# Performance work log

Measured on AMD Instinct MI355X. Metric: run time of the kernel, lower is better.

The kernel has to match this reference:

```python
import jax, jax.numpy as jnp
import numpy as np

N = 50000   # nodes
E = 800000  # edges (avg degree 16)
D = 128     # dim (in == out per layer)
R = 8       # num_relations
B = 4       # num_bases
L = 2       # conv_layer_num
EPS = 1e-5      # LayerNorm eps
SLOPE = 0.2     # leaky_relu negative slope


def setup_inputs() -> dict:
    key = jax.random.key(0)
    ks = jax.random.split(key, 10)
    s = 0.05
    x = jax.random.normal(ks[0], (N, D), dtype=jnp.float32)
    edge_index = jax.random.randint(ks[1], (2, E), 0, N)
    edge_type = jax.random.randint(ks[2], (E,), 0, R)
    basis = jax.random.normal(ks[3], (L, B, D, D), dtype=jnp.float32) * s
    att_r = jax.random.normal(ks[4], (L, R, B), dtype=jnp.float32) * s
    att = jax.random.normal(ks[5], (L, 2 * D), dtype=jnp.float32) * s
    root = jax.random.normal(ks[6], (L, D, D), dtype=jnp.float32) * s
    bias = jax.random.normal(ks[7], (L, D), dtype=jnp.float32) * s
    ln_w = jnp.ones((L, D), dtype=jnp.float32)
    ln_b = jnp.zeros((L, D), dtype=jnp.float32)
    return {"x": x, "edge_index": edge_index, "edge_type": edge_type,
            "basis": basis, "att_r": att_r, "att": att, "root": root,
            "bias": bias, "ln_w": ln_w, "ln_b": ln_b}


def _gnn_layer(x, src, dst, et, basis, att_r, att, root, bias, ln_w, ln_b):
    # relation weights from bases: [R, D, D]
    w = jnp.einsum('rb,bio->rio', att_r, basis)
    # transform all nodes under all relations once, then gather per edge
    xw = jnp.einsum('ni,rio->rno', x, w)          # [R, N, D]
    x_j = xw[et, src]                              # [E, D] relation-specific src msg
    xr = x @ root                                  # [N, D] root transform
    x_i = xr[dst]                                  # [E, D]
    # attention: (cat[x_i, x_j] * att).sum(-1), leaky_relu, segment softmax by dst
    alpha = x_i @ att[:D] + x_j @ att[D:]          # [E]
    alpha = jnp.where(alpha > 0, alpha, SLOPE * alpha)
    amax = jax.ops.segment_max(alpha, dst, num_segments=N)
    amax = jnp.where(jnp.isfinite(amax), amax, 0.0)
    ex = jnp.exp(alpha - amax[dst])
    denom = jax.ops.segment_sum(ex, dst, num_segments=N)
    alpha = ex / (denom[dst] + 1e-16)
    # weighted scatter-add aggregation (dropout rate = 0 -> identity)
    aggr = jax.ops.segment_sum(x_j * alpha[:, None], dst, num_segments=N)  # [N, D]
    out = aggr + xr + bias
    # LayerNorm
    mu = out.mean(-1, keepdims=True)
    var = out.var(-1, keepdims=True)
    out = (out - mu) / jnp.sqrt(var + EPS) * ln_w + ln_b
    return jnp.tanh(out)


def reference(x, edge_index, edge_type, basis, att_r, att, root, bias, ln_w, ln_b):
    src, dst = edge_index[0], edge_index[1]
    states = []
    for l in range(L):
        x = _gnn_layer(x, src, dst, edge_type, basis[l], att_r[l], att[l],
                       root[l], bias[l], ln_w[l], ln_b[l])
        states.append(x)
    return (x, jnp.stack(states))
```

## Files before the change

kernel.cpp:

```cpp
#include <hip/hip_runtime.h>
#include <math.h>

#define D 128
#define NB 4
#define NR 8
#define NLAYER 2
#define KTOT 640
#define EPSV 1e-5f
#define SLOPE 0.2f

typedef __attribute__((ext_vector_type(8))) short short8;
typedef __attribute__((ext_vector_type(4))) float f32x4;

__device__ __forceinline__ unsigned short f2bf(float f) {
  unsigned u = __float_as_uint(f);
  u += 0x7FFF + ((u >> 16) & 1);
  return (unsigned short)(u >> 16);
}

__device__ __forceinline__ float block_sum_128(float v, volatile float* scratch) {
#pragma unroll
  for (int off = 32; off > 0; off >>= 1) v += __shfl_xor(v, off);
  __syncthreads();
  if ((threadIdx.x & 63) == 0) scratch[threadIdx.x >> 6] = v;
  __syncthreads();
  return scratch[0] + scratch[1];
}

__global__ void hist_kernel(const int* __restrict__ dst, int* __restrict__ deg, int E) {
  int e = blockIdx.x * 256 + threadIdx.x;
  if (e < E) atomicAdd(&deg[dst[e]], 1);
}

__global__ void __launch_bounds__(1024) scan_kernel(const int* __restrict__ deg,
                                                    int* __restrict__ offs,
                                                    int* __restrict__ cur, int n) {
  __shared__ int wsums[16];
  const int tid = threadIdx.x, lane = tid & 63, wid = tid >> 6;
  int carry = 0;
  for (int base = 0; base < n; base += 4096) {
    int i0 = base + tid * 4;
    int v0 = 0, v1 = 0, v2 = 0, v3 = 0;
    if (i0 + 3 < n) {
      int4 q = *(const int4*)(deg + i0);
      v0 = q.x; v1 = q.y; v2 = q.z; v3 = q.w;
    } else if (i0 < n) {
      v0 = deg[i0];
      if (i0 + 1 < n) v1 = deg[i0 + 1];
      if (i0 + 2 < n) v2 = deg[i0 + 2];
    }
    int tsum = v0 + v1 + v2 + v3;
    int x = tsum;
#pragma unroll
    for (int off = 1; off < 64; off <<= 1) {
      int y = __shfl_up(x, off);
      if (lane >= off) x += y;
    }
    if (lane == 63) wsums[wid] = x;
    __syncthreads();
    if (wid == 0) {
      int ws = (lane < 16) ? wsums[lane] : 0;
#pragma unroll
      for (int off = 1; off < 16; off <<= 1) {
        int y = __shfl_up(ws, off);
        if (lane >= off) ws += y;
      }
      if (lane < 16) wsums[lane] = ws;
    }
    __syncthreads();
    int prefix = carry + ((wid > 0) ? wsums[wid - 1] : 0) + x - tsum;
    int e0 = prefix, e1 = e0 + v0, e2 = e1 + v1, e3 = e2 + v2;
    if (i0 < n)     { offs[i0] = e0;     cur[i0] = e0; }
    if (i0 + 1 < n) { offs[i0 + 1] = e1; cur[i0 + 1] = e1; }
    if (i0 + 2 < n) { offs[i0 + 2] = e2; cur[i0 + 2] = e2; }
    if (i0 + 3 < n) { offs[i0 + 3] = e3; cur[i0 + 3] = e3; }
    int btot = wsums[15];
    __syncthreads();
    carry += btot;
  }
  if (tid == 0) offs[n] = carry;
}

__global__ void scatter_kernel(const int* __restrict__ src, const int* __restrict__ dst,
                               const int* __restrict__ et, int* __restrict__ cur,
                               unsigned* __restrict__ csr, int E) {
  int e = blockIdx.x * 256 + threadIdx.x;
  if (e < E) {
    int d = dst[e];
    int pos = atomicAdd(&cur[d], 1);
    csr[pos] = (unsigned)src[e] | ((unsigned)et[e] << 16);
  }
}

__global__ void __launch_bounds__(128) prep_w(const float* __restrict__ basis,
                                              const float* __restrict__ root,
                                              const float* __restrict__ att,
                                              unsigned short* __restrict__ BT0,
                                              unsigned short* __restrict__ BT1,
                                              float* __restrict__ av0, float* __restrict__ av1) {
  __shared__ float scratch[2];
  int k = blockIdx.x, l = 0;
  if (k >= KTOT) { k -= KTOT; l = 1; }
  const float* basis_l = basis + (size_t)l * NB * D * D;
  const float* root_l  = root + (size_t)l * D * D;
  const float* att_l   = att + (size_t)l * 2 * D;
  unsigned short* BT = l ? BT1 : BT0;
  float* av = l ? av1 : av0;
  const int o = threadIdx.x;
  float v = (k < 512) ? basis_l[(size_t)(k >> 7) * (D * D) + (size_t)(k & 127) * D + o]
                      : root_l[(size_t)(k - 512) * D + o];
  BT[(size_t)o * KTOT + k] = f2bf(v);
  float w = (k < 512) ? att_l[D + o] : att_l[o];
  float s = block_sum_128(v * w, scratch);
  if (o == 0) av[k] = s;
}

__global__ void prep_x(const float* __restrict__ x0, unsigned short* __restrict__ ga, int N) {
  int n = blockIdx.x, c = threadIdx.x;
  float v = (n < N) ? x0[(size_t)n * D + c] : 0.f;
  ga[(size_t)n * KTOT + 512 + c] = f2bf(v);
}

__global__ void __launch_bounds__(256) a2_kernel(const unsigned short* __restrict__ ga,
                                                 const float* __restrict__ av,
                                                 float* __restrict__ ai,
                                                 float* __restrict__ ajb, int N) {
  int n = blockIdx.x * 4 + (threadIdx.x >> 6);
  int lane = threadIdx.x & 63;
  if (n >= N) return;
  unsigned xv = *(const unsigned*)(ga + (size_t)n * KTOT + 512 + 2 * lane);
  float x0 = __uint_as_float(xv << 16);
  float x1 = __uint_as_float(xv & 0xFFFF0000u);
  float d[5];
#pragma unroll
  for (int b = 0; b < 4; ++b) {
    float2 w = *(const float2*)(av + b * D + 2 * lane);
    d[b] = x0 * w.x + x1 * w.y;
  }
  {
    float2 w = *(const float2*)(av + 512 + 2 * lane);
    d[4] = x0 * w.x + x1 * w.y;
  }
#pragma unroll
  for (int off = 1; off < 64; off <<= 1) {
#pragma unroll
    for (int i = 0; i < 5; ++i) d[i] += __shfl_xor(d[i], off);
  }
  if (lane == 0) {
    *(float4*)(ajb + (size_t)n * 4) = make_float4(d[0], d[1], d[2], d[3]);
    ai[n] = d[4];
  }
}

__global__ void __launch_bounds__(256) node_flash(
    unsigned short* __restrict__ ga, const float* __restrict__ ai, const float* __restrict__ ajb,
    const int* __restrict__ offs, const unsigned* __restrict__ csr,
    const float* __restrict__ attr_l, int N) {
  __shared__ float s_c[NR * NB];
  __shared__ float4 s_wc[4][64];
  __shared__ unsigned s_pk[4][64];
  const int w = threadIdx.x >> 6, lane = threadIdx.x & 63;
  const int n = blockIdx.x * 4 + w;
  if (lane < NR * NB) s_c[lane] = attr_l[lane];
  if (n >= N) return;
  const int b0 = offs[n], b1 = offs[n + 1];
  const float ain = ai[n];
  float m = -INFINITY, ssum = 0.f;
  float acc[4][2] = {};
  for (int cb = b0; cb < b1; cb += 64) {
    int cnt = min(64, b1 - cb);
    float alpha = -INFINITY;
    unsigned pk = 0;
    float4 cv = make_float4(0.f, 0.f, 0.f, 0.f);
    if (lane < cnt) {
      pk = csr[cb + lane];
      unsigned sn = pk & 0xFFFFu, rt = pk >> 16;
      float4 aj = *(const float4*)(ajb + (size_t)sn * 4);
      cv = *(const float4*)(&s_c[rt * 4]);
      float a = ain + cv.x * aj.x + cv.y * aj.y + cv.z * aj.z + cv.w * aj.w;
      alpha = a > 0.f ? a : SLOPE * a;
    }
    float cmax = alpha;
#pragma unroll
    for (int off = 32; off > 0; off >>= 1) cmax = fmaxf(cmax, __shfl_xor(cmax, off));
    float nm = fmaxf(m, cmax);
    float ex = (lane < cnt) ? __expf(alpha - nm) : 0.f;
    float csum = ex;
#pragma unroll
    for (int off = 32; off > 0; off >>= 1) csum += __shfl_xor(csum, off);
    float f = __expf(m - nm);
    ssum = ssum * f + csum;
#pragma unroll
    for (int b = 0; b < 4; ++b) { acc[b][0] *= f; acc[b][1] *= f; }
    m = nm;
    s_pk[w][lane] = pk;
    s_wc[w][lane] = make_float4(ex * cv.x, ex * cv.y, ex * cv.z, ex * cv.w);
#pragma unroll 2
    for (int j = 0; j < cnt; ++j) {
      float4 wc = s_wc[w][j];
      unsigned sn = s_pk[w][j] & 0xFFFFu;
      unsigned xv = *(const unsigned*)(ga + (size_t)sn * KTOT + 512 + 2 * lane);
      float x0 = __uint_as_float(xv << 16);
      float x1 = __uint_as_float(xv & 0xFFFF0000u);
      acc[0][0] = fmaf(wc.x, x0, acc[0][0]); acc[0][1] = fmaf(wc.x, x1, acc[0][1]);
      acc[1][0] = fmaf(wc.y, x0, acc[1][0]); acc[1][1] = fmaf(wc.y, x1, acc[1][1]);
      acc[2][0] = fmaf(wc.z, x0, acc[2][0]); acc[2][1] = fmaf(wc.z, x1, acc[2][1]);
      acc[3][0] = fmaf(wc.w, x0, acc[3][0]); acc[3][1] = fmaf(wc.w, x1, acc[3][1]);
    }
  }
  float inv = 1.f / (ssum + 1e-16f);
  unsigned short* gp = ga + (size_t)n * KTOT;
#pragma unroll
  for (int b = 0; b < 4; ++b) {
    unsigned r = (unsigned)f2bf(acc[b][0] * inv) | ((unsigned)f2bf(acc[b][1] * inv) << 16);
    *(unsigned*)(gp + b * D + 2 * lane) = r;
  }
}

__global__ void __launch_bounds__(256) gemm2_kernel(
    unsigned short* __restrict__ ga, const unsigned short* __restrict__ BT,
    const float* __restrict__ bias_l, const float* __restrict__ lnw_l,
    const float* __restrict__ lnb_l, float* __restrict__ st,
    float* __restrict__ xfinal, int n_nodes) {
  __shared__ unsigned short sB[128 * 72];
  const int tid = threadIdx.x;
  const int wv = tid >> 6, lane = tid & 63;
  const int l15 = lane & 15, quad = lane >> 4;
  const int rowb = blockIdx.x * 64 + wv * 16;
  const unsigned short* garow = ga + (size_t)(rowb + l15) * KTOT;
  f32x4 acc[8];
  const f32x4 zero = {0.f, 0.f, 0.f, 0.f};
#pragma unroll
  for (int ct = 0; ct < 8; ++ct) acc[ct] = zero;
#pragma unroll
  for (int ch = 0; ch < 10; ++ch) {
    const int k0 = ch * 64;
    short8 a[2];
#pragma unroll
    for (int kc = 0; kc < 2; ++kc)
      a[kc] = *(const short8*)(garow + k0 + kc * 32 + quad * 8);
    __syncthreads();
#pragma unroll
    for (int p = 0; p < 4; ++p) {
      int idx = p * 256 + tid;
      int col = idx >> 3, k8 = idx & 7;
      *(short8*)(sB + col * 72 + k8 * 8) =
          *(const short8*)(BT + (size_t)col * KTOT + k0 + k8 * 8);
    }
    __syncthreads();
#pragma unroll
    for (int kc = 0; kc < 2; ++kc) {
#pragma unroll
      for (int ct = 0; ct < 8; ++ct) {
        const short8* b = (const short8*)(sB + (ct * 16 + l15) * 72 + kc * 32 + quad * 8);
        acc[ct] = __builtin_amdgcn_mfma_f32_16x16x32_bf16(a[kc], *b, acc[ct], 0, 0, 0);
      }
    }
  }
  const int r0 = rowb + quad * 4;
  float bia[8], lw[8], lb[8];
#pragma unroll
  for (int ct = 0; ct < 8; ++ct) {
    int col = ct * 16 + l15;
    bia[ct] = bias_l[col]; lw[ct] = lnw_l[col]; lb[ct] = lnb_l[col];
  }
  float vsum[4] = {0.f, 0.f, 0.f, 0.f}, vsq[4] = {0.f, 0.f, 0.f, 0.f};
#pragma unroll
  for (int ct = 0; ct < 8; ++ct) {
#pragma unroll
    for (int r = 0; r < 4; ++r) {
      float v = acc[ct][r] + bia[ct];
      acc[ct][r] = v;
      vsum[r] += v; vsq[r] += v * v;
    }
  }
#pragma unroll
  for (int r = 0; r < 4; ++r) {
#pragma unroll
    for (int off = 1; off < 16; off <<= 1) {
      vsum[r] += __shfl_xor(vsum[r], off);
      vsq[r]  += __shfl_xor(vsq[r], off);
    }
  }
  float mu[4], rs[4];
#pragma unroll
  for (int r = 0; r < 4; ++r) {
    mu[r] = vsum[r] * (1.0f / D);
    float var = vsq[r] * (1.0f / D) - mu[r] * mu[r];
    rs[r] = rsqrtf(var + EPSV);
  }
#pragma unroll
  for (int ct = 0; ct < 8; ++ct) {
#pragma unroll
    for (int r = 0; r < 4; ++r) {
      int row = r0 + r;
      if (row >= n_nodes) continue;
      int col = ct * 16 + l15;
      float nv = (acc[ct][r] - mu[r]) * rs[r] * lw[ct] + lb[ct];
      float val = tanhf(nv);
      st[(size_t)row * D + col] = val;
      if (xfinal) xfinal[(size_t)row * D + col] = val;
      ga[(size_t)row * KTOT + 512 + col] = f2bf(val);
    }
  }
}

extern "C" void kernel_launch(void* const* d_in, const int* in_sizes, int n_in,
                              void* d_out, int out_size, void* d_ws, size_t ws_size,
                              hipStream_t stream) {
  const float* x0    = (const float*)d_in[0];
  const int*   ei    = (const int*)d_in[1];
  const int*   etype = (const int*)d_in[2];
  const float* basis = (const float*)d_in[3];
  const float* att_r = (const float*)d_in[4];
  const float* att   = (const float*)d_in[5];
  const float* root  = (const float*)d_in[6];
  const float* bias  = (const float*)d_in[7];
  const float* lnw   = (const float*)d_in[8];
  const float* lnb   = (const float*)d_in[9];
  float* out = (float*)d_out;
  const int N = in_sizes[0] / D;
  const int E = in_sizes[2];
  const int Npad = ((N + 63) / 64) * 64;

  char* p = (char*)d_ws;
  auto alloc = [&](size_t bytes) { void* r = (void*)p; p += (bytes + 255) & ~(size_t)255; return r; };
  unsigned short* ga   = (unsigned short*)alloc((size_t)Npad * KTOT * 2);
  unsigned short* BT0  = (unsigned short*)alloc((size_t)D * KTOT * 2);
  unsigned short* BT1  = (unsigned short*)alloc((size_t)D * KTOT * 2);
  float*          av0  = (float*)alloc((size_t)KTOT * 4);
  float*          av1  = (float*)alloc((size_t)KTOT * 4);
  float*          ai   = (float*)alloc((size_t)N * 4);
  float*          ajb  = (float*)alloc((size_t)N * 4 * 4);
  int*            deg  = (int*)alloc((size_t)N * 4);
  int*            offs = (int*)alloc((size_t)(N + 1) * 4);
  int*            cur  = (int*)alloc((size_t)N * 4);
  unsigned*       csr  = (unsigned*)alloc((size_t)E * 4);

  const int* srcp = ei;
  const int* dstp = ei + E;

  hipMemsetAsync(deg, 0, (size_t)N * 4, stream);
  hist_kernel<<<(E + 255) / 256, 256, 0, stream>>>(dstp, deg, E);
  scan_kernel<<<1, 1024, 0, stream>>>(deg, offs, cur, N);
  scatter_kernel<<<(E + 255) / 256, 256, 0, stream>>>(srcp, dstp, etype, cur, csr, E);

  prep_w<<<2 * KTOT, 128, 0, stream>>>(basis, root, att, BT0, BT1, av0, av1);
  prep_x<<<Npad, 128, 0, stream>>>(x0, ga, N);

  float* states = out + (size_t)N * D;
  for (int l = 0; l < NLAYER; ++l) {
    const unsigned short* BT_l = l ? BT1 : BT0;
    const float* av_l = l ? av1 : av0;
    a2_kernel<<<(N + 3) / 4, 256, 0, stream>>>(ga, av_l, ai, ajb, N);
    node_flash<<<(N + 3) / 4, 256, 0, stream>>>(ga, ai, ajb, offs, csr,
                                                att_r + (size_t)l * NR * NB, N);
    float* st = states + (size_t)l * N * D;
    gemm2_kernel<<<Npad / 64, 256, 0, stream>>>(ga, BT_l, bias + (size_t)l * D,
                                                lnw + (size_t)l * D, lnb + (size_t)l * D,
                                                st, (l == NLAYER - 1) ? out : nullptr, N);
  }
}
```

Measured before the change: 442.6 us.

## Bucket edges before CSR scatter, fuse x prep with attention dots, widen GEMM blocks

Edge-to-CSR construction now goes through a two-pass path. A block-local bucketing kernel first groups edges by destination range into a staging buffer, and a second pass does the per-node atomic scatter, so the random atomics and writes have better locality. The input conversion kernel now also computes the first layer's attention dot products, which removes one a2 launch and a re-read of ga. The GEMM uses 512-thread blocks covering 128 rows, so each staged B tile in shared memory is reused by twice as many waves. In exchange it adds an 8-byte-per-edge staging buffer and an extra kernel pass, and each GEMM block now needs more registers.

```diff
diff --git a/kernel.cpp b/kernel.cpp
--- a/kernel.cpp
+++ b/kernel.cpp
@@ -8,6 +8,8 @@
 #define KTOT 640
 #define EPSV 1e-5f
 #define SLOPE 0.2f
+#define NBUK 32
+#define BSHIFT 11
 
 typedef __attribute__((ext_vector_type(8))) short short8;
 typedef __attribute__((ext_vector_type(4))) float f32x4;
@@ -34,7 +36,8 @@
 
 __global__ void __launch_bounds__(1024) scan_kernel(const int* __restrict__ deg,
                                                     int* __restrict__ offs,
-                                                    int* __restrict__ cur, int n) {
+                                                    int* __restrict__ cur,
+                                                    int* __restrict__ bcur, int n) {
   __shared__ int wsums[16];
   const int tid = threadIdx.x, lane = tid & 63, wid = tid >> 6;
   int carry = 0;
@@ -79,16 +82,45 @@
     carry += btot;
   }
   if (tid == 0) offs[n] = carry;
-}
-
-__global__ void scatter_kernel(const int* __restrict__ src, const int* __restrict__ dst,
-                               const int* __restrict__ et, int* __restrict__ cur,
-                               unsigned* __restrict__ csr, int E) {
+  __syncthreads();
+  if (tid < NBUK) {
+    int idx = tid << BSHIFT;
+    bcur[tid * 16] = offs[idx < n ? idx : n];
+  }
+}
+
+__global__ void __launch_bounds__(1024) bucket_kernel(
+    const int* __restrict__ src, const int* __restrict__ dst, const int* __restrict__ et,
+    int* __restrict__ bcur, unsigned long long* __restrict__ ebuf, int E) {
+  __shared__ int lcnt[NBUK];
+  __shared__ int lbase[NBUK];
+  const int tid = threadIdx.x;
+  const int e = blockIdx.x * 1024 + tid;
+  if (tid < NBUK) lcnt[tid] = 0;
+  __syncthreads();
+  int d = 0, b = 0, rank = 0;
+  unsigned pk = 0;
+  bool valid = e < E;
+  if (valid) {
+    d = dst[e];
+    pk = (unsigned)src[e] | ((unsigned)et[e] << 16);
+    b = d >> BSHIFT;
+    rank = atomicAdd(&lcnt[b], 1);
+  }
+  __syncthreads();
+  if (tid < NBUK && lcnt[tid] > 0) lbase[tid] = atomicAdd(&bcur[tid * 16], lcnt[tid]);
+  __syncthreads();
+  if (valid) ebuf[lbase[b] + rank] = ((unsigned long long)(unsigned)d << 32) | pk;
+}
+
+__global__ void scatter2_kernel(const unsigned long long* __restrict__ ebuf,
+                                int* __restrict__ cur, unsigned* __restrict__ csr, int E) {
   int e = blockIdx.x * 256 + threadIdx.x;
   if (e < E) {
-    int d = dst[e];
+    unsigned long long r = ebuf[e];
+    int d = (int)(r >> 32);
     int pos = atomicAdd(&cur[d], 1);
-    csr[pos] = (unsigned)src[e] | ((unsigned)et[e] << 16);
+    csr[pos] = (unsigned)r;
   }
 }
 
@@ -115,10 +147,40 @@
   if (o == 0) av[k] = s;
 }
 
-__global__ void prep_x(const float* __restrict__ x0, unsigned short* __restrict__ ga, int N) {
-  int n = blockIdx.x, c = threadIdx.x;
-  float v = (n < N) ? x0[(size_t)n * D + c] : 0.f;
-  ga[(size_t)n * KTOT + 512 + c] = f2bf(v);
+__global__ void __launch_bounds__(256) prep_xa(const float* __restrict__ x0,
+                                               const float* __restrict__ av,
+                                               unsigned short* __restrict__ ga,
+                                               float* __restrict__ ai,
+                                               float* __restrict__ ajb, int N, int Npad) {
+  int n = blockIdx.x * 4 + (threadIdx.x >> 6);
+  int lane = threadIdx.x & 63;
+  if (n >= Npad) return;
+  if (n >= N) {
+    *(unsigned*)(ga + (size_t)n * KTOT + 512 + 2 * lane) = 0;
+    return;
+  }
+  float2 xv = *(const float2*)(x0 + (size_t)n * D + 2 * lane);
+  unsigned packed = (unsigned)f2bf(xv.x) | ((unsigned)f2bf(xv.y) << 16);
+  *(unsigned*)(ga + (size_t)n * KTOT + 512 + 2 * lane) = packed;
+  float d[5];
+#pragma unroll
+  for (int b = 0; b < 4; ++b) {
+    float2 w = *(const float2*)(av + b * D + 2 * lane);
+    d[b] = xv.x * w.x + xv.y * w.y;
+  }
+  {
+    float2 w = *(const float2*)(av + 512 + 2 * lane);
+    d[4] = xv.x * w.x + xv.y * w.y;
+  }
+#pragma unroll
+  for (int off = 1; off < 64; off <<= 1) {
+#pragma unroll
+    for (int i = 0; i < 5; ++i) d[i] += __shfl_xor(d[i], off);
+  }
+  if (lane == 0) {
+    *(float4*)(ajb + (size_t)n * 4) = make_float4(d[0], d[1], d[2], d[3]);
+    ai[n] = d[4];
+  }
 }
 
 __global__ void __launch_bounds__(256) a2_kernel(const unsigned short* __restrict__ ga,
@@ -217,7 +279,7 @@
   }
 }
 
-__global__ void __launch_bounds__(256) gemm2_kernel(
+__global__ void __launch_bounds__(512) gemm2_kernel(
     unsigned short* __restrict__ ga, const unsigned short* __restrict__ BT,
     const float* __restrict__ bias_l, const float* __restrict__ lnw_l,
     const float* __restrict__ lnb_l, float* __restrict__ st,
@@ -226,7 +288,7 @@
   const int tid = threadIdx.x;
   const int wv = tid >> 6, lane = tid & 63;
   const int l15 = lane & 15, quad = lane >> 4;
-  const int rowb = blockIdx.x * 64 + wv * 16;
+  const int rowb = blockIdx.x * 128 + wv * 16;
   const unsigned short* garow = ga + (size_t)(rowb + l15) * KTOT;
   f32x4 acc[8];
   const f32x4 zero = {0.f, 0.f, 0.f, 0.f};
@@ -241,8 +303,8 @@
       a[kc] = *(const short8*)(garow + k0 + kc * 32 + quad * 8);
     __syncthreads();
 #pragma unroll
-    for (int p = 0; p < 4; ++p) {
-      int idx = p * 256 + tid;
+    for (int p = 0; p < 2; ++p) {
+      int idx = p * 512 + tid;
       int col = idx >> 3, k8 = idx & 7;
       *(short8*)(sB + col * 72 + k8 * 8) =
           *(const short8*)(BT + (size_t)col * KTOT + k0 + k8 * 8);
@@ -321,43 +383,46 @@
   float* out = (float*)d_out;
   const int N = in_sizes[0] / D;
   const int E = in_sizes[2];
-  const int Npad = ((N + 63) / 64) * 64;
+  const int Npad = ((N + 127) / 128) * 128;
 
   char* p = (char*)d_ws;
   auto alloc = [&](size_t bytes) { void* r = (void*)p; p += (bytes + 255) & ~(size_t)255; return r; };
-  unsigned short* ga   = (unsigned short*)alloc((size_t)Npad * KTOT * 2);
-  unsigned short* BT0  = (unsigned short*)alloc((size_t)D * KTOT * 2);
-  unsigned short* BT1  = (unsigned short*)alloc((size_t)D * KTOT * 2);
-  float*          av0  = (float*)alloc((size_t)KTOT * 4);
-  float*          av1  = (float*)alloc((size_t)KTOT * 4);
-  float*          ai   = (float*)alloc((size_t)N * 4);
-  float*          ajb  = (float*)alloc((size_t)N * 4 * 4);
-  int*            deg  = (int*)alloc((size_t)N * 4);
-  int*            offs = (int*)alloc((size_t)(N + 1) * 4);
-  int*            cur  = (int*)alloc((size_t)N * 4);
-  unsigned*       csr  = (unsigned*)alloc((size_t)E * 4);
+  unsigned short*     ga   = (unsigned short*)alloc((size_t)Npad * KTOT * 2);
+  unsigned short*     BT0  = (unsigned short*)alloc((size_t)D * KTOT * 2);
+  unsigned short*     BT1  = (unsigned short*)alloc((size_t)D * KTOT * 2);
+  float*              av0  = (float*)alloc((size_t)KTOT * 4);
+  float*              av1  = (float*)alloc((size_t)KTOT * 4);
+  float*              ai   = (float*)alloc((size_t)N * 4);
+  float*              ajb  = (float*)alloc((size_t)N * 4 * 4);
+  int*                deg  = (int*)alloc((size_t)N * 4);
+  int*                offs = (int*)alloc((size_t)(N + 1) * 4);
+  int*                cur  = (int*)alloc((size_t)N * 4);
+  int*                bcur = (int*)alloc((size_t)NBUK * 16 * 4);
+  unsigned*           csr  = (unsigned*)alloc((size_t)E * 4);
+  unsigned long long* ebuf = (unsigned long long*)alloc((size_t)E * 8);
 
   const int* srcp = ei;
   const int* dstp = ei + E;
 
   hipMemsetAsync(deg, 0, (size_t)N * 4, stream);
   hist_kernel<<<(E + 255) / 256, 256, 0, stream>>>(dstp, deg, E);
-  scan_kernel<<<1, 1024, 0, stream>>>(deg, offs, cur, N);
-  scatter_kernel<<<(E + 255) / 256, 256, 0, stream>>>(srcp, dstp, etype, cur, csr, E);
+  scan_kernel<<<1, 1024, 0, stream>>>(deg, offs, cur, bcur, N);
+  bucket_kernel<<<(E + 1023) / 1024, 1024, 0, stream>>>(srcp, dstp, etype, bcur, ebuf, E);
+  scatter2_kernel<<<(E + 255) / 256, 256, 0, stream>>>(ebuf, cur, csr, E);
 
   prep_w<<<2 * KTOT, 128, 0, stream>>>(basis, root, att, BT0, BT1, av0, av1);
-  prep_x<<<Npad, 128, 0, stream>>>(x0, ga, N);
+  prep_xa<<<Npad / 4, 256, 0, stream>>>(x0, av0, ga, ai, ajb, N, Npad);
 
   float* states = out + (size_t)N * D;
   for (int l = 0; l < NLAYER; ++l) {
     const unsigned short* BT_l = l ? BT1 : BT0;
-    const float* av_l = l ? av1 : av0;
-    a2_kernel<<<(N + 3) / 4, 256, 0, stream>>>(ga, av_l, ai, ajb, N);
+    if (l > 0)
+      a2_kernel<<<(N + 3) / 4, 256, 0, stream>>>(ga, av1, ai, ajb, N);
     node_flash<<<(N + 3) / 4, 256, 0, stream>>>(ga, ai, ajb, offs, csr,
                                                 att_r + (size_t)l * NR * NB, N);
     float* st = states + (size_t)l * N * D;
-    gemm2_kernel<<<Npad / 64, 256, 0, stream>>>(ga, BT_l, bias + (size_t)l * D,
-                                                lnw + (size_t)l * D, lnb + (size_t)l * D,
-                                                st, (l == NLAYER - 1) ? out : nullptr, N);
-  }
-}
+    gemm2_kernel<<<Npad / 128, 512, 0, stream>>>(ga, BT_l, bias + (size_t)l * D,
+                                                 lnw + (size_t)l * D, lnb + (size_t)l * D,
+                                                 st, (l == NLAYER - 1) ? out : nullptr, N);
+  }
+}
```

After: 418.3 us. 5.5% less time.
